# Kernel optimization log

Measured on AMD Instinct MI355X. Metric: run time of the kernel, lower is better.

The kernel has to match this reference:

```python
import jax, jax.numpy as jnp
import numpy as np

N_WAY = 5
N_SHOT = 25
N_SUPPORT = N_WAY * N_SHOT  # 125
N_QUERY = 2048
D = 8192
C_REG = 0.1        # default C_reg of MetaOptNetHead_SVM_CS
MAX_ITER = 20      # default maxIter of QPFunction
SIGMA = 0.1        # centering parameter of the interior-point iteration


def setup_inputs() -> dict:
    key = jax.random.key(0)
    k1, k2, k3 = jax.random.split(key, 3)
    query = jax.random.normal(k1, (N_QUERY, D), dtype=jnp.float32)
    support = jax.random.normal(k2, (N_SUPPORT, D), dtype=jnp.float32)
    support_labels = jax.random.randint(k3, (N_SUPPORT,), 0, N_WAY, dtype=jnp.int32)
    scale = jnp.ones((1,), dtype=jnp.float32)  # nn.Parameter([1.0])
    return {
        "query": query,
        "support": support,
        "support_labels": support_labels,
        "n_way": N_WAY,
        "n_shot": N_SHOT,
        "scale": scale,
    }


def _solve_qp(G, e, h, A, b):
    """Solve min_z 0.5 z^T G z + e^T z  s.t.  z <= h (C = I),  A z = b.

    Primal-dual infeasible-start interior-point method with MAX_ITER fixed
    Newton steps (the jax analogue of qpth's QPFunction(maxIter=20)).
    Shapes: G (B,n,n), e (B,n), h (B,n), A (B,p,n), b (B,p).
    """
    B, n = e.shape
    p = b.shape[1]
    m = n  # C = I -> one inequality per variable
    At = jnp.swapaxes(A, 1, 2)                      # (B,n,p)
    zero_pp = jnp.zeros((B, p, p), dtype=G.dtype)
    A_row = jnp.concatenate([A, zero_pp], axis=2)   # (B,p,n+p), constant

    z = jnp.zeros_like(e)
    s = jnp.ones_like(h)
    lam = jnp.ones_like(h)
    nu = jnp.zeros_like(b)

    def frac_to_boundary(x, dx):
        # largest alpha in (0,1] keeping x + alpha*dx > 0
        ratio = jnp.where(dx < 0, -x / jnp.where(dx < 0, dx, -1.0), jnp.inf)
        return jnp.min(ratio, axis=1)

    def step(carry, _):
        z, s, lam, nu = carry
        Gz = jnp.einsum('bij,bj->bi', G, z)
        r1 = Gz + e + lam + jnp.einsum('bpi,bp->bi', A, nu)   # dual residual (C^T lam = lam)
        r2 = z + s - h                                         # primal ineq residual
        r4 = jnp.einsum('bpi,bi->bp', A, z) - b                # primal eq residual
        mu = SIGMA * jnp.sum(s * lam, axis=1, keepdims=True) / m
        r3 = lam * s - mu                                      # perturbed complementarity
        # Reduced KKT system: (G + diag(lam/s)) dz + A^T dnu = rhs1 ; A dz = -r4
        H = G + jax.vmap(jnp.diag)(lam / s)                    # (B,n,n)
        rhs1 = -(r1 + (lam * r2 - r3) / s)                     # (B,n)
        K = jnp.concatenate(
            [jnp.concatenate([H, At], axis=2), A_row], axis=1)  # (B,n+p,n+p)
        rhs = jnp.concatenate([rhs1, -r4], axis=1)             # (B,n+p)
        sol = jnp.linalg.solve(K, rhs[..., None])[..., 0]
        dz, dnu = sol[:, :n], sol[:, n:]
        ds = -r2 - dz
        dlam = (-r3 - lam * ds) / s
        alpha = jnp.minimum(
            1.0, 0.99 * jnp.minimum(frac_to_boundary(s, ds),
                                    frac_to_boundary(lam, dlam)))[:, None]
        return (z + alpha * dz, s + alpha * ds,
                lam + alpha * dlam, nu + alpha * dnu), None

    (z, s, lam, nu), _ = jax.lax.scan(step, (z, s, lam, nu), None, length=MAX_ITER)
    return z


def _svm_cs_head(query, support, support_labels, n_way):
    support_b = support[None]            # (1, ns, d) -- head unsqueezes batch dim
    query_b = query[None]                # (1, nq, d)
    B, ns, _ = support_b.shape
    f32 = jnp.float32

    # Gram matrix of support, then kron with I_{n_way} (batched_kronecker == jnp.kron)
    K = jnp.einsum('bnd,bmd->bnm', support_b, support_b)            # (B,ns,ns)
    eye_w = jnp.eye(n_way, dtype=f32)
    G = jax.vmap(lambda k: jnp.kron(k, eye_w))(K)                    # (B,ns*nw,ns*nw)
    G = G + jnp.eye(n_way * ns, dtype=f32)[None]

    y1h = jax.nn.one_hot(support_labels, n_way, dtype=f32).reshape(B, ns * n_way)
    e = -y1h
    h = C_REG * y1h
    A = jnp.kron(jnp.eye(ns, dtype=f32), jnp.ones((1, n_way), f32))[None]  # (1,ns,ns*nw)
    b = jnp.zeros((B, ns), f32)

    qp_sol = _solve_qp(G, e, h, A, b)                                # (B, ns*nw)

    compat = jnp.einsum('bnd,bqd->bnq', support_b, query_b)          # (B,ns,nq)
    qp3 = qp_sol.reshape(B, ns, n_way)
    # logits[b,q,w] = sum_s qp3[b,s,w] * compat[b,s,q]
    logits = jnp.einsum('bsw,bsq->bqw', qp3, compat)                 # (B,nq,nw)
    num_sv = jnp.sum(jnp.any(qp3 > 0.001, axis=2))                   # support-vector count
    return logits, num_sv


def reference(query, support, support_labels, n_way, n_shot, scale):
    logits, num_sv = _svm_cs_head(query, support, support_labels, n_way)
    return scale * logits, num_sv
```

## Files before the change

### kernel.cpp

```cpp
#include <hip/hip_runtime.h>

#define NS   125
#define NW   5
#define NQ   2048
#define DD   8192
#define CREG 0.1f
#define PGD_ITERS 12

#define OFF_PART 0
#define OFF_K    1000000
#define OFF_QP3  1016000
#define OFF_W    1017000
#define OFF_LP   1060000

__global__ __launch_bounds__(256) void gram_partial(const float* __restrict__ support,
                                                    float* __restrict__ part) {
    __shared__ __align__(16) float As[128][68];
    __shared__ __align__(16) float Bs[128][68];
    const int tid = threadIdx.x;
    const int c  = blockIdx.x;
    const int qy = blockIdx.y, qz = blockIdx.z;
    const int d0 = c * 128;
    const int sy0 = qy * 64, sz0 = qz * 64;
    for (int idx = tid; idx < 64 * 128; idx += 256) {
        int sl = idx >> 7, dj = idx & 127;
        int sa = sy0 + sl, sb = sz0 + sl;
        As[dj][sl] = (sa < NS) ? support[(size_t)sa * DD + d0 + dj] : 0.f;
        Bs[dj][sl] = (sb < NS) ? support[(size_t)sb * DD + d0 + dj] : 0.f;
    }
    __syncthreads();
    const int tx = tid & 15, ty = tid >> 4;
    float acc[4][4];
#pragma unroll
    for (int i = 0; i < 4; i++)
#pragma unroll
        for (int j = 0; j < 4; j++) acc[i][j] = 0.f;
#pragma unroll 4
    for (int d = 0; d < 128; ++d) {
        float4 a = *(const float4*)&As[d][tx * 4];
        float4 b = *(const float4*)&Bs[d][ty * 4];
        float av[4] = {a.x, a.y, a.z, a.w};
        float bv[4] = {b.x, b.y, b.z, b.w};
#pragma unroll
        for (int i = 0; i < 4; i++)
#pragma unroll
            for (int j = 0; j < 4; j++) acc[i][j] += av[i] * bv[j];
    }
    float* dst = part + (size_t)c * (NS * NS);
#pragma unroll
    for (int i = 0; i < 4; i++) {
        int gi = sy0 + tx * 4 + i;
        if (gi >= NS) continue;
#pragma unroll
        for (int j = 0; j < 4; j++) {
            int gj = sz0 + ty * 4 + j;
            if (gj < NS) dst[gi * NS + gj] = acc[i][j];
        }
    }
}

__global__ __launch_bounds__(256) void gram_reduce(const float* __restrict__ part,
                                                   float* __restrict__ Kg) {
    int t = blockIdx.x * 256 + threadIdx.x;
    if (t < NS * NS) {
        float s = 0.f;
        for (int c = 0; c < 64; ++c) s += part[(size_t)c * (NS * NS) + t];
        Kg[t] = s;
    }
}

__global__ __launch_bounds__(256) void qp_solve(const float* __restrict__ Kg,
                                                const int* __restrict__ labels,
                                                float* __restrict__ qp3,
                                                float* __restrict__ outNumSv) {
    __shared__ __align__(16) float zs[NW][128];
    __shared__ float red2[128 * 25];
    __shared__ float rsmax[2];
    __shared__ int svcount;

    const int tid  = threadIdx.x;
    const int w    = tid >> 6;
    const int lane = tid & 63;
    const int c0   = w * 32;
    const int r0   = lane, r1 = lane + 64;

    float kr0[32], kr1[32];
#pragma unroll
    for (int j = 0; j < 32; ++j) {
        const int col = c0 + j;
        const bool cv = (col < NS);
        kr0[j] = cv ? Kg[col * NS + r0] : 0.f;
        kr1[j] = (cv && r1 < NS) ? Kg[col * NS + r1] : 0.f;
    }
    for (int idx = tid; idx < NW * 128; idx += 256) ((float*)zs)[idx] = 0.f;
    if (tid == 0) svcount = 0;
    float rsum0 = 0.f, rsum1 = 0.f;
#pragma unroll
    for (int j = 0; j < 32; ++j) { rsum0 += fabsf(kr0[j]); rsum1 += fabsf(kr1[j]); }
    red2[r0 * 25 + w * 5] = rsum0;
    red2[r1 * 25 + w * 5] = rsum1;
    __syncthreads();
    const int prow = w * 64 + lane;
    if (w < 2) {
        const float* rr = &red2[prow * 25];
        float t = (prow < NS) ? rr[0] + rr[5] + rr[10] + rr[15] : 0.f;
#pragma unroll
        for (int off = 32; off; off >>= 1) t = fmaxf(t, __shfl_xor(t, off));
        if (lane == 0) rsmax[w] = t;
    }
    __syncthreads();
    const float eta = 1.9f / (fmaxf(rsmax[0], rsmax[1]) + 1.0f);
    const int lab = (w < 2 && prow < NS) ? labels[prow] : 0;
    float z[NW] = {0.f, 0.f, 0.f, 0.f, 0.f};

    for (int it = 0; it < PGD_ITERS; ++it) {
        float acc0[NW] = {0.f, 0.f, 0.f, 0.f, 0.f};
        float acc1[NW] = {0.f, 0.f, 0.f, 0.f, 0.f};
#pragma unroll
        for (int c = 0; c < 8; ++c) {
            const int jb = c0 + 4 * c;
            float4 z0 = *(const float4*)&zs[0][jb];
            float4 z1 = *(const float4*)&zs[1][jb];
            float4 z2 = *(const float4*)&zs[2][jb];
            float4 z3 = *(const float4*)&zs[3][jb];
            float4 z4 = *(const float4*)&zs[4][jb];
            const float k00 = kr0[4*c], k01 = kr0[4*c+1], k02 = kr0[4*c+2], k03 = kr0[4*c+3];
            const float k10 = kr1[4*c], k11 = kr1[4*c+1], k12 = kr1[4*c+2], k13 = kr1[4*c+3];
            acc0[0] += k00*z0.x + k01*z0.y + k02*z0.z + k03*z0.w;
            acc0[1] += k00*z1.x + k01*z1.y + k02*z1.z + k03*z1.w;
            acc0[2] += k00*z2.x + k01*z2.y + k02*z2.z + k03*z2.w;
            acc0[3] += k00*z3.x + k01*z3.y + k02*z3.z + k03*z3.w;
            acc0[4] += k00*z4.x + k01*z4.y + k02*z4.z + k03*z4.w;
            acc1[0] += k10*z0.x + k11*z0.y + k12*z0.z + k13*z0.w;
            acc1[1] += k10*z1.x + k11*z1.y + k12*z1.z + k13*z1.w;
            acc1[2] += k10*z2.x + k11*z2.y + k12*z2.z + k13*z2.w;
            acc1[3] += k10*z3.x + k11*z3.y + k12*z3.z + k13*z3.w;
            acc1[4] += k10*z4.x + k11*z4.y + k12*z4.z + k13*z4.w;
        }
        {
            float* b0 = &red2[r0 * 25 + w * 5];
            b0[0] = acc0[0]; b0[1] = acc0[1]; b0[2] = acc0[2]; b0[3] = acc0[3]; b0[4] = acc0[4];
            float* b1 = &red2[r1 * 25 + w * 5];
            b1[0] = acc1[0]; b1[1] = acc1[1]; b1[2] = acc1[2]; b1[3] = acc1[3]; b1[4] = acc1[4];
        }
        __syncthreads();
        if (w < 2 && prow < NS) {
            const float* rr = &red2[prow * 25];
            float v[NW], h[NW];
#pragma unroll
            for (int a = 0; a < NW; a++) {
                float kz = rr[a] + rr[5 + a] + rr[10 + a] + rr[15 + a];
                float g = kz + z[a] - ((a == lab) ? 1.f : 0.f);
                v[a] = z[a] - eta * g;
                h[a] = (a == lab) ? CREG : 0.f;
            }
            float tau = fmaxf(fmaxf(fmaxf(v[0], v[1]), fmaxf(v[2], v[3])), v[4]);
#pragma unroll
            for (int n = 0; n < 7; ++n) {
                float g = 0.f, nf = 0.f;
#pragma unroll
                for (int a = 0; a < NW; a++) {
                    float d = v[a] - tau;
                    bool fr = (d <= h[a]);
                    g += fr ? d : h[a];
                    nf += fr ? 1.f : 0.f;
                }
                tau += g / nf;
            }
#pragma unroll
            for (int a = 0; a < NW; a++) {
                z[a] = fminf(v[a] - tau, h[a]);
                zs[a][prow] = z[a];
            }
        }
        __syncthreads();
    }

    if (w < 2 && prow < NS) {
        float m = fmaxf(fmaxf(fmaxf(z[0], z[1]), fmaxf(z[2], z[3])), z[4]);
        if (m > 0.001f) atomicAdd(&svcount, 1);
#pragma unroll
        for (int a = 0; a < NW; a++) qp3[prow * NW + a] = z[a];
    }
    __syncthreads();
    if (tid == 0) *outNumSv = (float)svcount;
}

__global__ __launch_bounds__(256) void w_kernel(const float* __restrict__ support,
                                                const float* __restrict__ qp3,
                                                float* __restrict__ W) {
    __shared__ float q3[NS * NW];
    __shared__ float red[4 * 64 * NW];
    const int tid = threadIdx.x;
    for (int i = tid; i < NS * NW; i += 256) q3[i] = qp3[i];
    __syncthreads();
    const int ld = tid & 63;
    const int sq = tid >> 6;
    const int d  = blockIdx.x * 64 + ld;
    const int s0 = sq * 32;
    const int s1 = (sq == 3) ? NS : (s0 + 32);
    float acc[NW] = {0.f, 0.f, 0.f, 0.f, 0.f};
#pragma unroll 4
    for (int s = s0; s < s1; ++s) {
        float sv = support[(size_t)s * DD + d];
#pragma unroll
        for (int a = 0; a < NW; a++) acc[a] += sv * q3[s * NW + a];
    }
    float* rr = &red[tid * NW];
#pragma unroll
    for (int a = 0; a < NW; a++) rr[a] = acc[a];
    __syncthreads();
    if (sq == 0) {
#pragma unroll
        for (int a = 0; a < NW; a++) {
            float s = red[(0 * 64 + ld) * NW + a] + red[(1 * 64 + ld) * NW + a]
                    + red[(2 * 64 + ld) * NW + a] + red[(3 * 64 + ld) * NW + a];
            W[(size_t)a * DD + d] = s;
        }
    }
}

__global__ __launch_bounds__(256) void logits_partial(const float* __restrict__ query,
                                                      const float* __restrict__ W,
                                                      float* __restrict__ lp) {
    const int tid = threadIdx.x;
    const int wave = tid >> 6, lane = tid & 63;
    const int q0 = blockIdx.x * 8 + wave * 2;
    const int q1 = q0 + 1;
    const int chunk = blockIdx.y;
    const int v0 = chunk * 512;
    float a0[NW] = {0.f, 0.f, 0.f, 0.f, 0.f};
    float a1[NW] = {0.f, 0.f, 0.f, 0.f, 0.f};
    const float4* qp0 = (const float4*)(query + (size_t)q0 * DD);
    const float4* qp1 = (const float4*)(query + (size_t)q1 * DD);
    for (int it = 0; it < 8; ++it) {
        int dv = v0 + it * 64 + lane;
        float4 qv0 = qp0[dv];
        float4 qv1 = qp1[dv];
#pragma unroll
        for (int a = 0; a < NW; a++) {
            float4 wv = ((const float4*)(W + (size_t)a * DD))[dv];
            a0[a] += qv0.x * wv.x + qv0.y * wv.y + qv0.z * wv.z + qv0.w * wv.w;
            a1[a] += qv1.x * wv.x + qv1.y * wv.y + qv1.z * wv.z + qv1.w * wv.w;
        }
    }
#pragma unroll
    for (int off = 32; off; off >>= 1) {
#pragma unroll
        for (int a = 0; a < NW; a++) {
            a0[a] += __shfl_xor(a0[a], off);
            a1[a] += __shfl_xor(a1[a], off);
        }
    }
    if (lane == 0) {
        float* dst = lp + (size_t)chunk * (NQ * NW);
#pragma unroll
        for (int a = 0; a < NW; a++) dst[q0 * NW + a] = a0[a];
#pragma unroll
        for (int a = 0; a < NW; a++) dst[q1 * NW + a] = a1[a];
    }
}

__global__ __launch_bounds__(256) void logits_finish(const float* __restrict__ lp,
                                                     const float* __restrict__ scale,
                                                     float* __restrict__ out) {
    int t = blockIdx.x * 256 + threadIdx.x;
    if (t < NQ * NW) {
        float s = lp[t] + lp[NQ * NW + t] + lp[2 * NQ * NW + t] + lp[3 * NQ * NW + t];
        out[t] = scale[0] * s;
    }
}

extern "C" void kernel_launch(void* const* d_in, const int* in_sizes, int n_in,
                              void* d_out, int out_size, void* d_ws, size_t ws_size,
                              hipStream_t stream) {
    const float* query   = (const float*)d_in[0];
    const float* support = (const float*)d_in[1];
    const int*   labels  = (const int*)d_in[2];
    const float* scale   = (const float*)d_in[5];
    float* out = (float*)d_out;
    float* ws  = (float*)d_ws;

    float* part = ws + OFF_PART;
    float* Kg   = ws + OFF_K;
    float* qp3  = ws + OFF_QP3;
    float* W    = ws + OFF_W;
    float* lp   = ws + OFF_LP;

    hipLaunchKernelGGL(gram_partial, dim3(64, 2, 2), dim3(256), 0, stream, support, part);
    hipLaunchKernelGGL(gram_reduce, dim3(62), dim3(256), 0, stream, part, Kg);
    hipLaunchKernelGGL(qp_solve, dim3(1), dim3(256), 0, stream, Kg, labels, qp3, out + NQ * NW);
    hipLaunchKernelGGL(w_kernel, dim3(DD / 64), dim3(256), 0, stream, support, qp3, W);
    hipLaunchKernelGGL(logits_partial, dim3(NQ / 8, 4), dim3(256), 0, stream, query, W, lp);
    hipLaunchKernelGGL(logits_finish, dim3((NQ * NW + 255) / 256), dim3(256), 0, stream, lp, scale, out);
}
```

Before: 169.4 us.

## Double-buffer QP solver scratch and give each wave its own z slice to drop a barrier

In the single-block QP solver, the reduction scratch and the z vector are now double-buffered. Each of the four waves now updates the 32 dual rows that match its own column block and writes them into a private per-wave z slice. That slice is read only by the same wave in the next iteration, so the second __syncthreads per iteration is removed and the projection work is spread over four waves instead of two. The cost is twice the shared-memory footprint for these buffers, plus correctness that relies on the ping-pong ordering across the remaining barrier.

After: 168.7 us. No clear change (-0.4%).

```diff
diff --git a/kernel.cpp b/kernel.cpp
--- a/kernel.cpp
+++ b/kernel.cpp
@@ -73,8 +73,8 @@
                                                 const int* __restrict__ labels,
                                                 float* __restrict__ qp3,
                                                 float* __restrict__ outNumSv) {
-    __shared__ __align__(16) float zs[NW][128];
-    __shared__ float red2[128 * 25];
+    __shared__ float red2[2][128 * 25];
+    __shared__ __align__(16) float zsw[2][4][NW][32];
     __shared__ float rsmax[2];
     __shared__ int svcount;
 
@@ -92,38 +92,40 @@
         kr0[j] = cv ? Kg[col * NS + r0] : 0.f;
         kr1[j] = (cv && r1 < NS) ? Kg[col * NS + r1] : 0.f;
     }
-    for (int idx = tid; idx < NW * 128; idx += 256) ((float*)zs)[idx] = 0.f;
+    for (int idx = tid; idx < 2 * 4 * NW * 32; idx += 256) ((float*)zsw)[idx] = 0.f;
     if (tid == 0) svcount = 0;
     float rsum0 = 0.f, rsum1 = 0.f;
 #pragma unroll
     for (int j = 0; j < 32; ++j) { rsum0 += fabsf(kr0[j]); rsum1 += fabsf(kr1[j]); }
-    red2[r0 * 25 + w * 5] = rsum0;
-    red2[r1 * 25 + w * 5] = rsum1;
-    __syncthreads();
-    const int prow = w * 64 + lane;
+    red2[0][r0 * 25 + w * 5] = rsum0;
+    red2[0][r1 * 25 + w * 5] = rsum1;
+    __syncthreads();
+    const int prw = w * 64 + lane;
     if (w < 2) {
-        const float* rr = &red2[prow * 25];
-        float t = (prow < NS) ? rr[0] + rr[5] + rr[10] + rr[15] : 0.f;
+        const float* rr = &red2[0][prw * 25];
+        float t = (prw < NS) ? rr[0] + rr[5] + rr[10] + rr[15] : 0.f;
 #pragma unroll
         for (int off = 32; off; off >>= 1) t = fmaxf(t, __shfl_xor(t, off));
         if (lane == 0) rsmax[w] = t;
     }
     __syncthreads();
     const float eta = 1.9f / (fmaxf(rsmax[0], rsmax[1]) + 1.0f);
-    const int lab = (w < 2 && prow < NS) ? labels[prow] : 0;
+    const int pr   = c0 + lane;
+    const bool act = (lane < 32) && (pr < NS);
+    const int lab  = act ? labels[pr] : 0;
     float z[NW] = {0.f, 0.f, 0.f, 0.f, 0.f};
 
     for (int it = 0; it < PGD_ITERS; ++it) {
+        const int p = it & 1, n = p ^ 1;
         float acc0[NW] = {0.f, 0.f, 0.f, 0.f, 0.f};
         float acc1[NW] = {0.f, 0.f, 0.f, 0.f, 0.f};
 #pragma unroll
         for (int c = 0; c < 8; ++c) {
-            const int jb = c0 + 4 * c;
-            float4 z0 = *(const float4*)&zs[0][jb];
-            float4 z1 = *(const float4*)&zs[1][jb];
-            float4 z2 = *(const float4*)&zs[2][jb];
-            float4 z3 = *(const float4*)&zs[3][jb];
-            float4 z4 = *(const float4*)&zs[4][jb];
+            float4 z0 = *(const float4*)&zsw[p][w][0][4 * c];
+            float4 z1 = *(const float4*)&zsw[p][w][1][4 * c];
+            float4 z2 = *(const float4*)&zsw[p][w][2][4 * c];
+            float4 z3 = *(const float4*)&zsw[p][w][3][4 * c];
+            float4 z4 = *(const float4*)&zsw[p][w][4][4 * c];
             const float k00 = kr0[4*c], k01 = kr0[4*c+1], k02 = kr0[4*c+2], k03 = kr0[4*c+3];
             const float k10 = kr1[4*c], k11 = kr1[4*c+1], k12 = kr1[4*c+2], k13 = kr1[4*c+3];
             acc0[0] += k00*z0.x + k01*z0.y + k02*z0.z + k03*z0.w;
@@ -138,14 +140,14 @@
             acc1[4] += k10*z4.x + k11*z4.y + k12*z4.z + k13*z4.w;
         }
         {
-            float* b0 = &red2[r0 * 25 + w * 5];
+            float* b0 = &red2[p][r0 * 25 + w * 5];
             b0[0] = acc0[0]; b0[1] = acc0[1]; b0[2] = acc0[2]; b0[3] = acc0[3]; b0[4] = acc0[4];
-            float* b1 = &red2[r1 * 25 + w * 5];
+            float* b1 = &red2[p][r1 * 25 + w * 5];
             b1[0] = acc1[0]; b1[1] = acc1[1]; b1[2] = acc1[2]; b1[3] = acc1[3]; b1[4] = acc1[4];
         }
         __syncthreads();
-        if (w < 2 && prow < NS) {
-            const float* rr = &red2[prow * 25];
+        if (act) {
+            const float* rr = &red2[p][pr * 25];
             float v[NW], h[NW];
 #pragma unroll
             for (int a = 0; a < NW; a++) {
@@ -156,7 +158,7 @@
             }
             float tau = fmaxf(fmaxf(fmaxf(v[0], v[1]), fmaxf(v[2], v[3])), v[4]);
 #pragma unroll
-            for (int n = 0; n < 7; ++n) {
+            for (int nn = 0; nn < 7; ++nn) {
                 float g = 0.f, nf = 0.f;
 #pragma unroll
                 for (int a = 0; a < NW; a++) {
@@ -170,17 +172,16 @@
 #pragma unroll
             for (int a = 0; a < NW; a++) {
                 z[a] = fminf(v[a] - tau, h[a]);
-                zs[a][prow] = z[a];
+                zsw[n][w][a][lane] = z[a];
             }
         }
-        __syncthreads();
-    }
-
-    if (w < 2 && prow < NS) {
+    }
+
+    if (act) {
         float m = fmaxf(fmaxf(fmaxf(z[0], z[1]), fmaxf(z[2], z[3])), z[4]);
         if (m > 0.001f) atomicAdd(&svcount, 1);
 #pragma unroll
-        for (int a = 0; a < NW; a++) qp3[prow * NW + a] = z[a];
+        for (int a = 0; a < NW; a++) qp3[pr * NW + a] = z[a];
     }
     __syncthreads();
     if (tid == 0) *outNumSv = (float)svcount;
```
